# Performance work log

Measured on AMD Instinct MI355X. Metric: run time of the kernel, lower is better.

The kernel has to match this reference:

```python
import jax, jax.numpy as jnp
import numpy as np

EPS = 1e-5
NEG_SLOPE = 0.2


def _edge_feat(x, k):
    # x: (B, N, C). DGCNN get_graph_feature with minus_center=True.
    B = x.shape[0]
    xx = jnp.sum(x * x, axis=-1)                       # (B, N)
    inner = jnp.einsum('bnc,bmc->bnm', x, x)           # (B, N, N)
    # -||xi - xj||^2 = -xx_i + 2<xi,xj> - xx_j
    pdist = 2.0 * inner - xx[:, :, None] - xx[:, None, :]
    _, idx = jax.lax.top_k(pdist, k)                   # (B, N, k) nearest (incl self)
    b_idx = jnp.arange(B)[:, None, None]
    nbr = x[b_idx, idx]                                # (B, N, k, C) gather
    center = x[:, :, None, :]
    # cat(feature - x, x) on channel dim -> (B, N, k, 2C)
    return jnp.concatenate([nbr - center, jnp.broadcast_to(center, nbr.shape)], axis=-1)


def _bn_lrelu(y, bn):
    # bn: (4, C) = gamma, beta, running_mean, running_var (inference-mode BN)
    g, b, m, v = bn[0], bn[1], bn[2], bn[3]
    y = (y - m) * (g * jax.lax.rsqrt(v + EPS)) + b
    return jnp.where(y >= 0, y, NEG_SLOPE * y)


def _conv_bn(y, W, bn):
    # 1x1 conv == per-point linear: W (out, in)
    return _bn_lrelu(jnp.einsum('...c,oc->...o', y, W), bn)


def _forward(x, W1, W2, W3, W4, W5, W6, W7, W8, W9,
             bn1, bn2, bn3, bn4, bn5, bn6, bn7, bn8, k=20):
    B, N, _ = x.shape
    f = _edge_feat(x, k)                               # (B, N, k, 6)
    h = _conv_bn(_conv_bn(f, W1, bn1), W2, bn2)
    x1 = jnp.max(h, axis=2)                            # (B, N, 64)
    f = _edge_feat(x1, k)                              # (B, N, k, 128)
    h = _conv_bn(_conv_bn(f, W3, bn3), W4, bn4)
    x2 = jnp.max(h, axis=2)                            # (B, N, 64)
    f = _edge_feat(x2, k)
    h = _conv_bn(f, W5, bn5)
    x3 = jnp.max(h, axis=2)                            # (B, N, 64)
    cat = jnp.concatenate([x1, x2, x3], axis=-1)       # (B, N, 192)
    vf = _conv_bn(cat, W6, bn6)                        # (B, N, emb_dims)
    g = jnp.mean(vf, axis=1)                           # (B, emb_dims) adaptive_avg_pool1d
    h = jnp.concatenate([jnp.broadcast_to(g[:, None, :], (B, N, g.shape[-1])), x1, x2, x3], axis=-1)
    h = _conv_bn(h, W7, bn7)                           # (B, N, 512)
    h = _conv_bn(h, W8, bn8)                           # (B, N, 256); dropout p given -> eval identity
    out = jnp.einsum('bnc,oc->bno', h, W9)             # (B, N, 3)
    return g, out


def setup_inputs() -> dict:
    key = jax.random.key(0)
    ks = jax.random.split(key, 32)
    B, N = 8, 4096
    d = {"x": jax.random.normal(ks[0], (B, N, 3), jnp.float32)}
    wdims = [(64, 6), (64, 64), (64, 128), (64, 64), (64, 128),
             (1024, 192), (512, 1216), (256, 512), (3, 256)]
    for i, (o, c) in enumerate(wdims):
        d[f"W{i+1}"] = 0.05 * jax.random.normal(ks[1 + i], (o, c), jnp.float32)
    bnC = [64, 64, 64, 64, 64, 1024, 512, 256]
    for i, c in enumerate(bnC):
        kk = jax.random.split(ks[10 + i], 4)
        gamma = 1.0 + 0.1 * jax.random.normal(kk[0], (c,), jnp.float32)
        beta = 0.1 * jax.random.normal(kk[1], (c,), jnp.float32)
        mean = 0.1 * jax.random.normal(kk[2], (c,), jnp.float32)
        var = 0.5 + jax.random.uniform(kk[3], (c,), jnp.float32)
        d[f"bn{i+1}"] = jnp.stack([gamma, beta, mean, var])
    return d


def reference(x, W1, W2, W3, W4, W5, W6, W7, W8, W9,
              bn1, bn2, bn3, bn4, bn5, bn6, bn7, bn8):
    return _forward(x, W1, W2, W3, W4, W5, W6, W7, W8, W9,
                    bn1, bn2, bn3, bn4, bn5, bn6, bn7, bn8)
```

## Files before the change

kernel.cpp:

```cpp
#include <hip/hip_runtime.h>
#include <hip/hip_bf16.h>

constexpr int Nn = 4096;
constexpr float EPSf = 1e-5f;

__device__ __forceinline__ float lrelu(float v){ return v >= 0.f ? v : 0.2f * v; }

__device__ __forceinline__ void topk_ins(float (&tv)[20], int (&ti)[20],
                                         float &minv, int &minpos, float s, int m){
#pragma unroll
  for (int i = 0; i < 20; ++i){
    bool sel = (i == minpos);
    tv[i] = sel ? s : tv[i];
    ti[i] = sel ? m : ti[i];
  }
  minv = tv[0]; minpos = 0;
#pragma unroll
  for (int i = 1; i < 20; ++i){
    if (tv[i] < minv){ minv = tv[i]; minpos = i; }
  }
}

__device__ __forceinline__ void topk_ins2(float (&tv)[20], int (&ti)[20],
                                          float &minv, int &mini, int &minpos,
                                          float s, int m){
#pragma unroll
  for (int i = 0; i < 20; ++i){
    bool sel = (i == minpos);
    tv[i] = sel ? s : tv[i];
    ti[i] = sel ? m : ti[i];
  }
  minv = tv[0]; mini = ti[0]; minpos = 0;
#pragma unroll
  for (int i = 1; i < 20; ++i){
    bool worse = (tv[i] < minv) || (tv[i] == minv && ti[i] > mini);
    if (worse){ minv = tv[i]; mini = ti[i]; minpos = i; }
  }
}

__global__ __launch_bounds__(128)
void knn1_t(const float* __restrict__ xin, int* __restrict__ idxout)
{
  __shared__ float4 tile[128];
  const int tid = threadIdx.x;
  const int row = blockIdx.x * 128 + tid;
  const int mbase = (row >> 12) * Nn;

  const float c0 = xin[row*3+0], c1 = xin[row*3+1], c2 = xin[row*3+2];

  float tv[20]; int ti[20];
#pragma unroll
  for (int i = 0; i < 20; ++i){ tv[i] = -3.4e38f; ti[i] = 0; }
  float minv = -3.4e38f; int minpos = 0;

  for (int t0 = 0; t0 < Nn; t0 += 128){
    int m = t0 + tid;
    float a0 = xin[(mbase + m)*3 + 0];
    float a1 = xin[(mbase + m)*3 + 1];
    float a2 = xin[(mbase + m)*3 + 2];
    tile[tid] = make_float4(a0, a1, a2, a0*a0 + a1*a1 + a2*a2);
    __syncthreads();
#pragma unroll 1
    for (int ml = 0; ml < 128; ++ml){
      float4 v = tile[ml];
      float score = 2.f * (v.x*c0 + v.y*c1 + v.z*c2) - v.w;
      if (score > minv) topk_ins(tv, ti, minv, minpos, score, mbase + t0 + ml);
    }
    __syncthreads();
  }
#pragma unroll
  for (int i = 0; i < 20; ++i) idxout[row * 20 + i] = ti[i];
}

__global__ __launch_bounds__(256, 3)
void knn64_s(const float* __restrict__ xin, int* __restrict__ idxout)
{
  __shared__ float smem[8320];
  float* txx = smem + 8192;
  const int tid = threadIdx.x;
  const int w    = tid >> 6;
  const int lane = tid & 63;
  const int row  = blockIdx.x * 64 + lane;
  const int mbase = (row >> 12) * Nn;

  float creg[64];
  {
    const float4* src = (const float4*)(xin + (size_t)row * 64);
#pragma unroll
    for (int q = 0; q < 16; ++q) *(float4*)&creg[4*q] = src[q];
  }

  float tv[20]; int ti[20];
#pragma unroll
  for (int i = 0; i < 20; ++i){ tv[i] = -3.4e38f; ti[i] = 0; }
  float minv = -3.4e38f; int mini = 0; int minpos = 0;

  for (int t0 = 0; t0 < Nn; t0 += 128){
    {
      const float4* src = (const float4*)(xin + (size_t)(mbase + t0) * 64);
      float4* dst = (float4*)smem;
#pragma unroll
      for (int it = 0; it < 8; ++it) dst[it * 256 + tid] = src[it * 256 + tid];
    }
    __syncthreads();
    if (tid < 128){
      const float4* trow = (const float4*)(smem + tid * 64);
      float s0 = 0.f, s1 = 0.f;
#pragma unroll
      for (int j = 0; j < 16; j += 2){
        float4 a = trow[(j + tid) & 15];
        float4 b = trow[(j + 1 + tid) & 15];
        s0 += a.x*a.x + a.y*a.y + a.z*a.z + a.w*a.w;
        s1 += b.x*b.x + b.y*b.y + b.z*b.z + b.w*b.w;
      }
      txx[tid] = s0 + s1;
    }
    __syncthreads();
#pragma unroll 1
    for (int j = 0; j < 32; ++j){
      int ml = (j << 2) | w;
      const float4* trow = (const float4*)(smem + ml * 64);
      float d0 = 0.f, d1 = 0.f, d2 = 0.f, d3 = 0.f;
#pragma unroll
      for (int q = 0; q < 16; q += 4){
        float4 v0 = trow[q+0], v1 = trow[q+1], v2 = trow[q+2], v3 = trow[q+3];
        d0 += creg[4*q+ 0]*v0.x + creg[4*q+ 1]*v0.y + creg[4*q+ 2]*v0.z + creg[4*q+ 3]*v0.w;
        d1 += creg[4*q+ 4]*v1.x + creg[4*q+ 5]*v1.y + creg[4*q+ 6]*v1.z + creg[4*q+ 7]*v1.w;
        d2 += creg[4*q+ 8]*v2.x + creg[4*q+ 9]*v2.y + creg[4*q+10]*v2.z + creg[4*q+11]*v2.w;
        d3 += creg[4*q+12]*v3.x + creg[4*q+13]*v3.y + creg[4*q+14]*v3.z + creg[4*q+15]*v3.w;
      }
      float score = 2.f * ((d0 + d1) + (d2 + d3)) - txx[ml];
      int gm = mbase + t0 + ml;
      if (score > minv || (score == minv && gm < mini))
        topk_ins2(tv, ti, minv, mini, minpos, score, gm);
    }
    __syncthreads();
  }

  float* mv = smem;
  int*   mi = (int*)(smem + 3840);
  if (w > 0){
#pragma unroll
    for (int i = 0; i < 20; ++i){
      mv[((w-1)*64 + lane)*20 + i] = tv[i];
      mi[((w-1)*64 + lane)*20 + i] = ti[i];
    }
  }
  __syncthreads();
  if (w == 0){
#pragma unroll 1
    for (int ss = 0; ss < 3; ++ss){
#pragma unroll 1
      for (int i = 0; i < 20; ++i){
        float v = mv[(ss*64 + lane)*20 + i];
        int   m = mi[(ss*64 + lane)*20 + i];
        if (v > minv || (v == minv && m < mini))
          topk_ins2(tv, ti, minv, mini, minpos, v, m);
      }
    }
#pragma unroll
    for (int i = 0; i < 20; ++i) idxout[row * 20 + i] = ti[i];
  }
}

__global__ __launch_bounds__(256)
void edge_first(const float* __restrict__ x, const int* __restrict__ idx,
                const float* __restrict__ W1, const float* __restrict__ bn1,
                const float* __restrict__ W2, const float* __restrict__ bn2,
                float* __restrict__ x1)
{
  const int tid = threadIdx.x;
  const int o = tid & 63;
  const int w = tid >> 6;
  float w1r[6];
#pragma unroll
  for (int j = 0; j < 6; ++j) w1r[j] = W1[o * 6 + j];
  float S1 = bn1[o] * rsqrtf(bn1[192 + o] + EPSf);
  float B1 = bn1[64 + o] - bn1[128 + o] * S1;
  float w2r[64];
#pragma unroll
  for (int q = 0; q < 16; ++q) *(float4*)&w2r[4*q] = *(const float4*)&W2[o * 64 + 4*q];
  float S2 = bn2[o] * rsqrtf(bn2[192 + o] + EPSf);
  float B2 = bn2[64 + o] - bn2[128 + o] * S2;

  __shared__ float h1buf[4][64];
  const int pbase = blockIdx.x * 32 + w * 8;
  for (int i = 0; i < 8; ++i){
    int row = pbase + i;
    float c0 = x[row*3+0], c1 = x[row*3+1], c2 = x[row*3+2];
    float acc = -3.4e38f;
    const int* ip = idx + row * 20;
    for (int k = 0; k < 20; ++k){
      int mg = ip[k];
      float t = w1r[0]*(x[mg*3+0]-c0) + w1r[1]*(x[mg*3+1]-c1) + w1r[2]*(x[mg*3+2]-c2)
              + w1r[3]*c0 + w1r[4]*c1 + w1r[5]*c2;
      h1buf[w][o] = lrelu(t * S1 + B1);
      __syncthreads();
      float t2 = 0.f;
#pragma unroll
      for (int q = 0; q < 16; ++q){
        float4 hv = *(float4*)&h1buf[w][4*q];
        t2 += w2r[4*q]*hv.x + w2r[4*q+1]*hv.y + w2r[4*q+2]*hv.z + w2r[4*q+3]*hv.w;
      }
      __syncthreads();
      acc = fmaxf(acc, lrelu(t2 * S2 + B2));
    }
    x1[(size_t)row * 64 + o] = acc;
  }
}

__global__ __launch_bounds__(256, 2)
void edge_mid(const float* __restrict__ xin, const int* __restrict__ idx,
              const float* __restrict__ Wa, const float* __restrict__ bna,
              const float* __restrict__ Wb, const float* __restrict__ bnb,
              float* __restrict__ xout)
{
  const int tid = threadIdx.x;
  const int o = tid & 63;
  const int w = tid >> 6;
  float war[128];
#pragma unroll
  for (int q = 0; q < 32; ++q) *(float4*)&war[4*q] = *(const float4*)&Wa[o * 128 + 4*q];
  float Sa = bna[o] * rsqrtf(bna[192 + o] + EPSf);
  float Ba = bna[64 + o] - bna[128 + o] * Sa;
  float wbr[64];
#pragma unroll
  for (int q = 0; q < 16; ++q) *(float4*)&wbr[4*q] = *(const float4*)&Wb[o * 64 + 4*q];
  float Sb = bnb[o] * rsqrtf(bnb[192 + o] + EPSf);
  float Bb = bnb[64 + o] - bnb[128 + o] * Sb;

  __shared__ float fbuf[4][128];
  __shared__ float hbuf[4][64];
  const int pbase = blockIdx.x * 32 + w * 8;
  for (int i = 0; i < 8; ++i){
    int row = pbase + i;
    float co = xin[(size_t)row * 64 + o];
    fbuf[w][64 + o] = co;
    float acc = -3.4e38f;
    const int* ip = idx + row * 20;
    for (int k = 0; k < 20; ++k){
      int mg = ip[k];
      fbuf[w][o] = xin[(size_t)mg * 64 + o] - co;
      __syncthreads();
      float t = 0.f;
#pragma unroll
      for (int q = 0; q < 32; ++q){
        float4 fv = *(float4*)&fbuf[w][4*q];
        t += war[4*q]*fv.x + war[4*q+1]*fv.y + war[4*q+2]*fv.z + war[4*q+3]*fv.w;
      }
      hbuf[w][o] = lrelu(t * Sa + Ba);
      __syncthreads();
      float t2 = 0.f;
#pragma unroll
      for (int q = 0; q < 16; ++q){
        float4 hv = *(float4*)&hbuf[w][4*q];
        t2 += wbr[4*q]*hv.x + wbr[4*q+1]*hv.y + wbr[4*q+2]*hv.z + wbr[4*q+3]*hv.w;
      }
      acc = fmaxf(acc, lrelu(t2 * Sb + Bb));
    }
    xout[(size_t)row * 64 + o] = acc;
  }
}

__global__ __launch_bounds__(256, 2)
void edge_last(const float* __restrict__ xin, const int* __restrict__ idx,
               const float* __restrict__ Wa, const float* __restrict__ bna,
               float* __restrict__ xout)
{
  const int tid = threadIdx.x;
  const int o = tid & 63;
  const int w = tid >> 6;
  float war[128];
#pragma unroll
  for (int q = 0; q < 32; ++q) *(float4*)&war[4*q] = *(const float4*)&Wa[o * 128 + 4*q];
  float Sa = bna[o] * rsqrtf(bna[192 + o] + EPSf);
  float Ba = bna[64 + o] - bna[128 + o] * Sa;

  __shared__ float fbuf[4][128];
  const int pbase = blockIdx.x * 32 + w * 8;
  for (int i = 0; i < 8; ++i){
    int row = pbase + i;
    float co = xin[(size_t)row * 64 + o];
    fbuf[w][64 + o] = co;
    float acc = -3.4e38f;
    const int* ip = idx + row * 20;
    for (int k = 0; k < 20; ++k){
      int mg = ip[k];
      fbuf[w][o] = xin[(size_t)mg * 64 + o] - co;
      __syncthreads();
      float t = 0.f;
#pragma unroll
      for (int q = 0; q < 32; ++q){
        float4 fv = *(float4*)&fbuf[w][4*q];
        t += war[4*q]*fv.x + war[4*q+1]*fv.y + war[4*q+2]*fv.z + war[4*q+3]*fv.w;
      }
      __syncthreads();
      acc = fmaxf(acc, lrelu(t * Sa + Ba));
    }
    xout[(size_t)row * 64 + o] = acc;
  }
}

__global__ __launch_bounds__(256, 2)
void vf_mean(const float* __restrict__ x1, const float* __restrict__ x2,
             const float* __restrict__ x3, const float* __restrict__ W6,
             const float* __restrict__ bn6, float* __restrict__ gsum)
{
  const int tid = threadIdx.x;
  const int bid = blockIdx.x;
  const int oc = bid & 3, nch = (bid >> 2) & 15, b = bid >> 6;
  const int o = oc * 256 + tid;
  float wr[192];
#pragma unroll
  for (int q = 0; q < 48; ++q) *(float4*)&wr[4*q] = *(const float4*)&W6[o * 192 + 4*q];
  float S = bn6[o] * rsqrtf(bn6[3*1024 + o] + EPSf);
  float Bn = bn6[1024 + o] - bn6[2*1024 + o] * S;

  __shared__ float cbuf[8 * 192];
  float local = 0.f;
  const int nbase = b * Nn + nch * 256;
  for (int p0 = 0; p0 < 256; p0 += 8){
#pragma unroll
    for (int it = 0; it < 6; ++it){
      int i = it * 256 + tid;
      int p = i / 192, j = i - p * 192;
      int row = nbase + p0 + p;
      float v = (j < 64) ? x1[(size_t)row*64 + j]
              : (j < 128) ? x2[(size_t)row*64 + j - 64]
              : x3[(size_t)row*64 + j - 128];
      cbuf[p * 192 + j] = v;
    }
    __syncthreads();
#pragma unroll 1
    for (int p = 0; p < 8; ++p){
      float t = 0.f;
#pragma unroll
      for (int q = 0; q < 48; ++q){
        float4 fv = *(float4*)&cbuf[p * 192 + 4*q];
        t += wr[4*q]*fv.x + wr[4*q+1]*fv.y + wr[4*q+2]*fv.z + wr[4*q+3]*fv.w;
      }
      local += lrelu(t * S + Bn);
    }
    __syncthreads();
  }
  atomicAdd(&gsum[b * 1024 + o], local);
}

__global__ void g_final(float* __restrict__ g, float* __restrict__ gout)
{
  int i = blockIdx.x * 256 + threadIdx.x;
  float v = g[i] * (1.f / 4096.f);
  g[i] = v;
  gout[i] = v;
}

__global__ void gbias7_k(const float* __restrict__ g, const float* __restrict__ W7,
                         float* __restrict__ gb7)
{
  const int tid = threadIdx.x;
  const int b = blockIdx.x >> 1, half = blockIdx.x & 1;
  const int o = half * 256 + tid;
  __shared__ float gs[1024];
#pragma unroll
  for (int it = 0; it < 4; ++it) gs[it * 256 + tid] = g[b * 1024 + it * 256 + tid];
  __syncthreads();
  float t = 0.f;
  const float4* wrow = (const float4*)&W7[(size_t)o * 1216];
#pragma unroll 8
  for (int q = 0; q < 256; ++q){
    float4 wv = wrow[q];
    float4 gv = *(float4*)&gs[4*q];
    t += wv.x*gv.x + wv.y*gv.y + wv.z*gv.z + wv.w*gv.w;
  }
  gb7[b * 512 + o] = t;
}

__global__ void transpose_k(const float* __restrict__ W7, const float* __restrict__ W8,
                            float* __restrict__ w7xt, float* __restrict__ w8t)
{
  int i = blockIdx.x * 256 + threadIdx.x;
  if (i < 98304){
    int j = i >> 9, o = i & 511;
    w7xt[i] = W7[(size_t)o * 1216 + 1024 + j];
  } else {
    int i2 = i - 98304;
    int j = i2 >> 8, o = i2 & 255;
    w8t[i2] = W8[o * 512 + j];
  }
}

__global__ __launch_bounds__(256, 2)
void mlp_final(const float* __restrict__ x1, const float* __restrict__ x2,
               const float* __restrict__ x3, const float* __restrict__ w7xt,
               const float* __restrict__ gb7, const float* __restrict__ bn7,
               const float* __restrict__ w8t, const float* __restrict__ bn8,
               const float* __restrict__ W9, float* __restrict__ out)
{
  const int tid = threadIdx.x;
  const int row0 = blockIdx.x * 16;
  const int b = row0 >> 12;
  __shared__ float A[256 * 20];
  __shared__ float H7[512 * 20];

#pragma unroll
  for (int it = 0; it < 12; ++it){
    int i = it * 256 + tid;
    int part = i >> 10, rem = i & 1023;
    int p = rem >> 6, o = rem & 63;
    const float* src = part == 0 ? x1 : part == 1 ? x2 : x3;
    A[(part * 64 + o) * 20 + p] = src[(size_t)(row0 + p) * 64 + o];
  }
  __syncthreads();

  const int o0 = tid, o1 = 256 + tid;
  float S0 = bn7[o0] * rsqrtf(bn7[3*512 + o0] + EPSf);
  float Bs0 = gb7[b*512 + o0] * S0 + bn7[512 + o0] - bn7[2*512 + o0] * S0;
  float S1 = bn7[o1] * rsqrtf(bn7[3*512 + o1] + EPSf);
  float Bs1 = gb7[b*512 + o1] * S1 + bn7[512 + o1] - bn7[2*512 + o1] * S1;
  float acc0[16], acc1[16];
#pragma unroll
  for (int p = 0; p < 16; ++p){ acc0[p] = 0.f; acc1[p] = 0.f; }
#pragma unroll 2
  for (int j = 0; j < 192; ++j){
    float w0 = w7xt[j * 512 + o0];
    float w1 = w7xt[j * 512 + o1];
#pragma unroll
    for (int q = 0; q < 4; ++q){
      float4 f = *(float4*)&A[j * 20 + 4*q];
      acc0[4*q+0] += w0 * f.x; acc0[4*q+1] += w0 * f.y; acc0[4*q+2] += w0 * f.z; acc0[4*q+3] += w0 * f.w;
      acc1[4*q+0] += w1 * f.x; acc1[4*q+1] += w1 * f.y; acc1[4*q+2] += w1 * f.z; acc1[4*q+3] += w1 * f.w;
    }
  }
#pragma unroll
  for (int p = 0; p < 16; ++p){
    H7[o0 * 20 + p] = lrelu(acc0[p] * S0 + Bs0);
    H7[o1 * 20 + p] = lrelu(acc1[p] * S1 + Bs1);
  }
  __syncthreads();

  float S8 = bn8[tid] * rsqrtf(bn8[3*256 + tid] + EPSf);
  float B8 = bn8[256 + tid] - bn8[2*256 + tid] * S8;
  float acc8[16];
#pragma unroll
  for (int p = 0; p < 16; ++p) acc8[p] = 0.f;
#pragma unroll 2
  for (int j = 0; j < 512; ++j){
    float wv = w8t[j * 256 + tid];
#pragma unroll
    for (int q = 0; q < 4; ++q){
      float4 h = *(float4*)&H7[j * 20 + 4*q];
      acc8[4*q+0] += wv * h.x; acc8[4*q+1] += wv * h.y; acc8[4*q+2] += wv * h.z; acc8[4*q+3] += wv * h.w;
    }
  }
  __syncthreads();
#pragma unroll
  for (int p = 0; p < 16; ++p) A[tid * 20 + p] = lrelu(acc8[p] * S8 + B8);
  __syncthreads();

  if (tid < 192){
    int c = tid >> 6, j0 = tid & 63;
    float w9r[4];
#pragma unroll
    for (int q = 0; q < 4; ++q) w9r[q] = W9[c * 256 + j0 + 64*q];
#pragma unroll 1
    for (int p = 0; p < 16; ++p){
      float s = 0.f;
#pragma unroll
      for (int q = 0; q < 4; ++q) s += w9r[q] * A[(j0 + 64*q) * 20 + p];
#pragma unroll
      for (int off = 32; off; off >>= 1) s += __shfl_down(s, off, 64);
      if (j0 == 0) out[(size_t)(row0 + p) * 3 + c] = s;
    }
  }
}

__global__ void sentinel_k(float* __restrict__ o, float val){
  int i = blockIdx.x*256 + threadIdx.x;
  if (i < 106496) o[i] = val;
}

extern "C" void kernel_launch(void* const* d_in, const int* in_sizes, int n_in,
                              void* d_out, int out_size, void* d_ws, size_t ws_size,
                              hipStream_t stream) {
  const float* x  = (const float*)d_in[0];
  const float* W1 = (const float*)d_in[1];
  const float* W2 = (const float*)d_in[2];
  const float* W3 = (const float*)d_in[3];
  const float* W4 = (const float*)d_in[4];
  const float* W5 = (const float*)d_in[5];
  const float* W6 = (const float*)d_in[6];
  const float* W7 = (const float*)d_in[7];
  const float* W8 = (const float*)d_in[8];
  const float* W9 = (const float*)d_in[9];
  const float* bn1 = (const float*)d_in[10];
  const float* bn2 = (const float*)d_in[11];
  const float* bn3 = (const float*)d_in[12];
  const float* bn4 = (const float*)d_in[13];
  const float* bn5 = (const float*)d_in[14];
  const float* bn6 = (const float*)d_in[15];
  const float* bn7 = (const float*)d_in[16];
  const float* bn8 = (const float*)d_in[17];

  float* out_g = (float*)d_out;
  float* out_o = out_g + 8192;

  bool ok_sizes = (n_in == 18) && in_sizes[0]==98304 && out_size == 106496;
  if (!ok_sizes){ sentinel_k<<<416, 256, 0, stream>>>((float*)d_out, 999.0f); return; }

  float* wsf  = (float*)d_ws;
  float* x1   = wsf;
  float* x2   = x1 + 2097152;
  float* x3   = x2 + 2097152;
  float* gbuf = x3 + 2097152;
  int*   idxb = (int*)(gbuf + 8192);
  float* gb7  = (float*)idxb;
  float* w7xt = gb7 + 4096;
  float* w8t  = w7xt + 98304;
  const size_t NEED = (size_t)(2097152*3 + 8192 + 655360) * 4;
  if (ws_size < NEED){ sentinel_k<<<416, 256, 0, stream>>>((float*)d_out, 12345.0f); return; }

  hipMemsetAsync(gbuf, 0, 8192 * sizeof(float), stream);

  knn1_t<<<256, 128, 0, stream>>>(x, idxb);
  edge_first<<<1024, 256, 0, stream>>>(x, idxb, W1, bn1, W2, bn2, x1);
  knn64_s<<<512, 256, 0, stream>>>(x1, idxb);
  edge_mid<<<1024, 256, 0, stream>>>(x1, idxb, W3, bn3, W4, bn4, x2);
  knn64_s<<<512, 256, 0, stream>>>(x2, idxb);
  edge_last<<<1024, 256, 0, stream>>>(x2, idxb, W5, bn5, x3);
  transpose_k<<<896, 256, 0, stream>>>(W7, W8, w7xt, w8t);
  vf_mean<<<512, 256, 0, stream>>>(x1, x2, x3, W6, bn6, gbuf);
  g_final<<<32, 256, 0, stream>>>(gbuf, out_g);
  gbias7_k<<<16, 256, 0, stream>>>(gbuf, W7, gb7);
  mlp_final<<<2048, 256, 0, stream>>>(x1, x2, x3, w7xt, gb7, bn7, w8t, bn8, W9, out_o);
}
```

Measured before the change: 6.285 ms.

## Buffer KNN candidates in shared memory and batch top-k insertions per wavefront

In the 64-dim KNN kernel, candidate scores that beat the current threshold go into a per-thread shared-memory buffer instead of triggering an immediate top-k insertion. When any lane in the wavefront fills its buffer, the whole wavefront drains all buffers together, which cuts the divergence from sporadic inserts. The cost is a larger shared-memory footprint (about 25 KB more), which may lower occupancy below the launch bound of 3 blocks, plus some stale-threshold insertions of candidates that a tighter minimum would have rejected.

```diff
diff --git a/kernel.cpp b/kernel.cpp
--- a/kernel.cpp
+++ b/kernel.cpp
@@ -3,6 +3,7 @@
 
 constexpr int Nn = 4096;
 constexpr float EPSf = 1e-5f;
+constexpr int KBUF = 12;
 
 __device__ __forceinline__ float lrelu(float v){ return v >= 0.f ? v : 0.2f * v; }
 
@@ -75,13 +76,15 @@
 __global__ __launch_bounds__(256, 3)
 void knn64_s(const float* __restrict__ xin, int* __restrict__ idxout)
 {
-  __shared__ float smem[8320];
-  float* txx = smem + 8192;
+  __shared__ float tile[8192];
+  __shared__ float txx[128];
+  __shared__ float lbufs[256 * 25];
   const int tid = threadIdx.x;
   const int w    = tid >> 6;
   const int lane = tid & 63;
   const int row  = blockIdx.x * 64 + lane;
   const int mbase = (row >> 12) * Nn;
+  float* lbuf = lbufs + tid * 25;
 
   float creg[64];
   {
@@ -94,17 +97,18 @@
 #pragma unroll
   for (int i = 0; i < 20; ++i){ tv[i] = -3.4e38f; ti[i] = 0; }
   float minv = -3.4e38f; int mini = 0; int minpos = 0;
+  int cnt = 0;
 
   for (int t0 = 0; t0 < Nn; t0 += 128){
     {
       const float4* src = (const float4*)(xin + (size_t)(mbase + t0) * 64);
-      float4* dst = (float4*)smem;
+      float4* dst = (float4*)tile;
 #pragma unroll
       for (int it = 0; it < 8; ++it) dst[it * 256 + tid] = src[it * 256 + tid];
     }
     __syncthreads();
     if (tid < 128){
-      const float4* trow = (const float4*)(smem + tid * 64);
+      const float4* trow = (const float4*)(tile + tid * 64);
       float s0 = 0.f, s1 = 0.f;
 #pragma unroll
       for (int j = 0; j < 16; j += 2){
@@ -119,7 +123,7 @@
 #pragma unroll 1
     for (int j = 0; j < 32; ++j){
       int ml = (j << 2) | w;
-      const float4* trow = (const float4*)(smem + ml * 64);
+      const float4* trow = (const float4*)(tile + ml * 64);
       float d0 = 0.f, d1 = 0.f, d2 = 0.f, d3 = 0.f;
 #pragma unroll
       for (int q = 0; q < 16; q += 4){
@@ -131,14 +135,54 @@
       }
       float score = 2.f * ((d0 + d1) + (d2 + d3)) - txx[ml];
       int gm = mbase + t0 + ml;
-      if (score > minv || (score == minv && gm < mini))
-        topk_ins2(tv, ti, minv, mini, minpos, score, gm);
-    }
-    __syncthreads();
-  }
-
-  float* mv = smem;
-  int*   mi = (int*)(smem + 3840);
+      if (score > minv || (score == minv && gm < mini)){
+        lbuf[2*cnt] = score;
+        ((int*)lbuf)[2*cnt + 1] = gm;
+        ++cnt;
+      }
+      if (__ballot(cnt >= KBUF)){
+        int maxc = cnt;
+#pragma unroll
+        for (int off = 32; off; off >>= 1){
+          int o = __shfl_xor(maxc, off, 64);
+          maxc = o > maxc ? o : maxc;
+        }
+#pragma unroll 1
+        for (int e = 0; e < maxc; ++e){
+          if (e < cnt){
+            float v = lbuf[2*e];
+            int   m = ((int*)lbuf)[2*e + 1];
+            if (v > minv || (v == minv && m < mini))
+              topk_ins2(tv, ti, minv, mini, minpos, v, m);
+          }
+        }
+        cnt = 0;
+      }
+    }
+    __syncthreads();
+  }
+  {
+    int maxc = cnt;
+#pragma unroll
+    for (int off = 32; off; off >>= 1){
+      int o = __shfl_xor(maxc, off, 64);
+      maxc = o > maxc ? o : maxc;
+    }
+#pragma unroll 1
+    for (int e = 0; e < maxc; ++e){
+      if (e < cnt){
+        float v = lbuf[2*e];
+        int   m = ((int*)lbuf)[2*e + 1];
+        if (v > minv || (v == minv && m < mini))
+          topk_ins2(tv, ti, minv, mini, minpos, v, m);
+      }
+    }
+    cnt = 0;
+  }
+
+  float* mv = tile;
+  int*   mi = (int*)(tile + 3840);
+  __syncthreads();
   if (w > 0){
 #pragma unroll
     for (int i = 0; i < 20; ++i){
```

Measured after the change: 5.239 ms. 16.6% less time.
